# Performance work log

Measured on AMD Instinct MI355X. Metric: run time of the kernel, lower is better.

## Reference

```python
import jax, jax.numpy as jnp
import numpy as np
import math

B, S, DIM = 1, 2048, 1024
H, KVH = 16, 4
HD = DIM // H            # 64
KV_DIM = KVH * HD        # 256


def setup_inputs() -> dict:
    key = jax.random.key(0)
    ks = jax.random.split(key, 8)
    std = 0.02
    return {
        "x": jax.random.normal(ks[0], (B, S, DIM), jnp.float32),
        "Wq": jax.random.normal(ks[1], (DIM, DIM), jnp.float32) * std,
        "Wk": jax.random.normal(ks[2], (KV_DIM, DIM), jnp.float32) * std,
        "Wv": jax.random.normal(ks[3], (KV_DIM, DIM), jnp.float32) * std,
        "Wg": jax.random.normal(ks[4], (KV_DIM, DIM), jnp.float32) * std,
        "Wo": jax.random.normal(ks[5], (DIM, DIM), jnp.float32) * std,
        "q_gain": jnp.full((H,), 1.0, jnp.float32),
        "lambda_param": jnp.full((H,), 0.5, jnp.float32),
    }


def _rms_norm(x):
    eps = jnp.finfo(x.dtype).eps
    return x * jax.lax.rsqrt(jnp.mean(x * x, axis=-1, keepdims=True) + eps)


def _polar_rotary(seq_len, head_dim, dtype):
    # PolarRotary: angles = arange(0, d, 2)/d * pi; radius decays with position
    angles = jnp.arange(0, head_dim, 2, dtype=jnp.float32) / head_dim * math.pi
    pos = jnp.arange(seq_len, dtype=jnp.float32)
    radius = 1.0 / (1.0 + pos[:, None] * 0.01)          # [S, 1]
    ang = pos[:, None] * angles[None, :]                 # [S, d/2]
    cos = (radius * jnp.cos(ang)).astype(dtype)          # [S, d/2]
    sin = (radius * jnp.sin(ang)).astype(dtype)
    return cos[None, None], sin[None, None]              # [1,1,S,d/2]


def _apply_rotary(x, cos, sin):
    half = x.shape[-1] // 2
    x1, x2 = x[..., :half], x[..., half:]
    return jnp.concatenate([x1 * cos + x2 * sin, x1 * -sin + x2 * cos], axis=-1)


def _causal_attn(q, k, v, scale, mask):
    # q,k,v: [B,H,S,d]
    s = jnp.einsum("bhqd,bhkd->bhqk", q, k) * scale
    s = jnp.where(mask, s, jnp.finfo(s.dtype).min)
    p = jax.nn.softmax(s, axis=-1)
    return jnp.einsum("bhqk,bhkd->bhqd", p, v)


def reference(x, Wq, Wk, Wv, Wg, Wo, q_gain, lambda_param):
    bsz, seqlen, dim = x.shape
    q = (x @ Wq.T).reshape(bsz, seqlen, H, HD).transpose(0, 2, 1, 3)      # [B,H,S,d]
    k = (x @ Wk.T).reshape(bsz, seqlen, KVH, HD).transpose(0, 2, 1, 3)    # [B,KVH,S,d]
    v = (x @ Wv.T).reshape(bsz, seqlen, KVH, HD).transpose(0, 2, 1, 3)

    # value gate (VGA)
    v_g = jax.nn.sigmoid((x @ Wg.T).reshape(bsz, seqlen, KVH, HD).transpose(0, 2, 1, 3))
    v = v * v_g

    q = _rms_norm(q)
    k = _rms_norm(k)

    cos, sin = _polar_rotary(seqlen, HD, q.dtype)
    q = _apply_rotary(q, cos, sin)
    k = _apply_rotary(k, cos, sin)

    q = q * q_gain.astype(q.dtype)[None, :, None, None]

    # GQA: repeat kv heads
    rep = H // KVH
    k = jnp.repeat(k, rep, axis=1)
    v = jnp.repeat(v, rep, axis=1)

    # differential attention: split head dim in halves
    half = HD // 2
    q1, q2 = q[..., :half], q[..., half:]
    k1, k2 = k[..., :half], k[..., half:]
    v1, v2 = v[..., :half], v[..., half:]

    scale = 1.0 / math.sqrt(half)
    mask = jnp.tril(jnp.ones((seqlen, seqlen), dtype=bool))[None, None]
    a1 = _causal_attn(q1, k1, v1, scale, mask)
    a2 = _causal_attn(q2, k2, v2, scale, mask)

    lp = lambda_param.astype(q.dtype)[None, :, None, None]
    y = jnp.concatenate([a1 - lp * a2, a1 + lp * a2], axis=-1)            # [B,H,S,d]
    y = y.transpose(0, 2, 1, 3).reshape(bsz, seqlen, dim)
    return y @ Wo.T
```

## Files before the change

kernel.cpp:

```cpp
#include <hip/hip_runtime.h>
#include <hip/hip_bf16.h>
#include <math.h>

#define S_LEN 2048
#define DIM   1024
#define NH    16
#define NKVH  4
#define HD    64
#define KVDIM 256

typedef __hip_bfloat16 bf16;
typedef __attribute__((ext_vector_type(8))) short short8;
typedef __attribute__((ext_vector_type(4))) float f32x4;

#define GLOBAL_AS __attribute__((address_space(1)))
#define LDS_AS    __attribute__((address_space(3)))

__device__ __forceinline__ void gload_lds16(const bf16* g, bf16* l) {
    __builtin_amdgcn_global_load_lds((const GLOBAL_AS void*)g, (LDS_AS void*)l,
                                     16, 0, 0);
}

__global__ __launch_bounds__(256) void cast6(
    const float* __restrict__ x,  const float* __restrict__ Wq,
    const float* __restrict__ Wk, const float* __restrict__ Wv,
    const float* __restrict__ Wg, const float* __restrict__ Wo,
    bf16* __restrict__ xb,  bf16* __restrict__ Wqb,
    bf16* __restrict__ Wkb, bf16* __restrict__ Wvb,
    bf16* __restrict__ Wgb, bf16* __restrict__ Wob,
    float* __restrict__ rc, float* __restrict__ rs) {
    if (blockIdx.y == 6) {
        const int idx = blockIdx.x * 256 + threadIdx.x;
        if (idx < S_LEN * 32) {
            const int s = idx >> 5, i = idx & 31;
            float af  = (float)(((double)(2 * i) / 64.0) * 3.14159265358979323846);
            float ang = (float)s * af;
            float radius = 1.0f / (1.0f + 0.01f * (float)s);
            rc[idx] = radius * (float)cos((double)ang);
            rs[idx] = radius * (float)sin((double)ang);
        }
        return;
    }
    const float* s; bf16* d; int n;
    switch (blockIdx.y) {
        case 0: s = x;  d = xb;  n = S_LEN * DIM; break;
        case 1: s = Wq; d = Wqb; n = DIM * DIM;   break;
        case 2: s = Wk; d = Wkb; n = KVDIM * DIM; break;
        case 3: s = Wv; d = Wvb; n = KVDIM * DIM; break;
        case 4: s = Wg; d = Wgb; n = KVDIM * DIM; break;
        default: s = Wo; d = Wob; n = DIM * DIM;  break;
    }
    for (int i = (blockIdx.x * 256 + threadIdx.x) * 4; i < n; i += gridDim.x * 1024) {
        float4 v = *(const float4*)(s + i);
        d[i]     = __float2bfloat16(v.x);
        d[i + 1] = __float2bfloat16(v.y);
        d[i + 2] = __float2bfloat16(v.z);
        d[i + 3] = __float2bfloat16(v.w);
    }
}

__device__ __forceinline__ void gemm_core(
    const bf16* __restrict__ A, const bf16* __restrict__ B,
    float* __restrict__ C, int bm, int bn, int N, int K) {
    __shared__ bf16 As[64 * 64];
    __shared__ bf16 Bs[64 * 64];
    const int tid  = threadIdx.x;
    const int w    = tid >> 6;
    const int lane = tid & 63;
    const int quad = lane >> 4;
    const int lm   = lane & 15;
    const int srow = tid >> 3;
    const int sseg = (tid & 7) ^ (srow & 7);
    const bf16* a0p = A + (size_t)(bm + srow) * K + (sseg << 3);
    const bf16* a1p = a0p + (size_t)32 * K;
    const bf16* b0p = B + (size_t)(bn + srow) * K + (sseg << 3);
    const bf16* b1p = b0p + (size_t)32 * K;
    bf16* ldsA = As + w * 512;
    bf16* ldsB = Bs + w * 512;

    f32x4 acc[4] = {};
    const int ra  = w * 16 + lm;
    const int rax = ra & 7;
    const int aoff0 = ra * 64 + (((quad    ) ^ rax) << 3);
    const int aoff1 = ra * 64 + (((quad + 4) ^ rax) << 3);
    const int rbx = lm & 7;
    const int boff0 = lm * 64 + (((quad    ) ^ rbx) << 3);
    const int boff1 = lm * 64 + (((quad + 4) ^ rbx) << 3);

    for (int k0 = 0; k0 < K; k0 += 64) {
        gload_lds16(a0p + k0, ldsA);
        gload_lds16(a1p + k0, ldsA + 2048);
        gload_lds16(b0p + k0, ldsB);
        gload_lds16(b1p + k0, ldsB + 2048);
        __syncthreads();
        short8 a0 = *(const short8*)&As[aoff0];
        short8 a1 = *(const short8*)&As[aoff1];
        #pragma unroll
        for (int t = 0; t < 4; ++t) {
            short8 b0 = *(const short8*)&Bs[boff0 + t * 16 * 64];
            short8 b1 = *(const short8*)&Bs[boff1 + t * 16 * 64];
            acc[t] = __builtin_amdgcn_mfma_f32_16x16x32_bf16(a0, b0, acc[t], 0, 0, 0);
            acc[t] = __builtin_amdgcn_mfma_f32_16x16x32_bf16(a1, b1, acc[t], 0, 0, 0);
        }
        __syncthreads();
    }
    const int r0 = bm + w * 16 + quad * 4;
    #pragma unroll
    for (int t = 0; t < 4; ++t) {
        const int col = bn + t * 16 + lm;
        #pragma unroll
        for (int i = 0; i < 4; ++i)
            C[(size_t)(r0 + i) * N + col] = acc[t][i];
    }
}

__global__ __launch_bounds__(256) void gemm_out(
    const bf16* __restrict__ Yb, const bf16* __restrict__ Wob,
    float* __restrict__ C) {
    gemm_core(Yb, Wob, C, blockIdx.y * 64, blockIdx.x * 64, DIM, DIM);
}

__global__ __launch_bounds__(256) void gemm_qkvg_post(
    const bf16* __restrict__ xb,  const bf16* __restrict__ Wqb,
    const bf16* __restrict__ Wkb, const bf16* __restrict__ Wvb,
    const bf16* __restrict__ Wgb,
    bf16* __restrict__ Qb, bf16* __restrict__ Kpk, bf16* __restrict__ Vpk,
    const float* __restrict__ qgain,
    const float* __restrict__ rc, const float* __restrict__ rs) {
    __shared__ bf16 As[64 * 64];
    __shared__ bf16 Bs[64 * 64];
    __shared__ bf16 Gs[64 * 64];
    const int cx = blockIdx.x;
    const int bm = blockIdx.y * 64;
    const int tid  = threadIdx.x;
    const int w    = tid >> 6;
    const int lane = tid & 63;
    const int quad = lane >> 4;
    const int lm   = lane & 15;
    const int srow = tid >> 3;
    const int sseg = (tid & 7) ^ (srow & 7);

    int mode, bn;
    const bf16 *B0, *B1;
    if (cx < 4)      { mode = 2; bn = cx * 64;        B0 = Wvb; B1 = Wgb; }
    else if (cx < 8) { mode = 1; bn = (cx - 4) * 64;  B0 = Wkb; B1 = Wkb; }
    else             { mode = 0; bn = (cx - 8) * 64;  B0 = Wqb; B1 = Wqb; }

    const bf16* a0p = xb + (size_t)(bm + srow) * DIM + (sseg << 3);
    const bf16* a1p = a0p + (size_t)32 * DIM;
    const bf16* b0p = B0 + (size_t)(bn + srow) * DIM + (sseg << 3);
    const bf16* b1p = b0p + (size_t)32 * DIM;
    const bf16* g0p = B1 + (size_t)(bn + srow) * DIM + (sseg << 3);
    const bf16* g1p = g0p + (size_t)32 * DIM;
    bf16* ldsA = As + w * 512;
    bf16* ldsB = Bs + w * 512;
    bf16* ldsG = Gs + w * 512;

    f32x4 acc[4]  = {};
    f32x4 acc2[4] = {};
    const int ra  = w * 16 + lm;
    const int rax = ra & 7;
    const int aoff0 = ra * 64 + (((quad    ) ^ rax) << 3);
    const int aoff1 = ra * 64 + (((quad + 4) ^ rax) << 3);
    const int rbx = lm & 7;
    const int boff0 = lm * 64 + (((quad    ) ^ rbx) << 3);
    const int boff1 = lm * 64 + (((quad + 4) ^ rbx) << 3);

    for (int k0 = 0; k0 < DIM; k0 += 64) {
        gload_lds16(a0p + k0, ldsA);
        gload_lds16(a1p + k0, ldsA + 2048);
        gload_lds16(b0p + k0, ldsB);
        gload_lds16(b1p + k0, ldsB + 2048);
        if (mode == 2) {
            gload_lds16(g0p + k0, ldsG);
            gload_lds16(g1p + k0, ldsG + 2048);
        }
        __syncthreads();
        short8 a0 = *(const short8*)&As[aoff0];
        short8 a1 = *(const short8*)&As[aoff1];
        #pragma unroll
        for (int t = 0; t < 4; ++t) {
            short8 b0 = *(const short8*)&Bs[boff0 + t * 16 * 64];
            short8 b1 = *(const short8*)&Bs[boff1 + t * 16 * 64];
            acc[t] = __builtin_amdgcn_mfma_f32_16x16x32_bf16(a0, b0, acc[t], 0, 0, 0);
            acc[t] = __builtin_amdgcn_mfma_f32_16x16x32_bf16(a1, b1, acc[t], 0, 0, 0);
        }
        if (mode == 2) {
            #pragma unroll
            for (int t = 0; t < 4; ++t) {
                short8 g0 = *(const short8*)&Gs[boff0 + t * 16 * 64];
                short8 g1 = *(const short8*)&Gs[boff1 + t * 16 * 64];
                acc2[t] = __builtin_amdgcn_mfma_f32_16x16x32_bf16(a0, g0, acc2[t], 0, 0, 0);
                acc2[t] = __builtin_amdgcn_mfma_f32_16x16x32_bf16(a1, g1, acc2[t], 0, 0, 0);
            }
        }
        __syncthreads();
    }

    const int r0 = bm + w * 16 + quad * 4;
    if (mode == 2) {
        const int kvh = cx;
        #pragma unroll
        for (int t = 0; t < 4; ++t) {
            const int d = t * 16 + lm;
            const int half = d >> 5, d32 = d & 31;
            #pragma unroll
            for (int i = 0; i < 4; ++i) {
                const int s = r0 + i;
                float val = acc[t][i] / (1.0f + __expf(-acc2[t][i]));
                const size_t vi = (((((size_t)(kvh*2 + half)*64 + (s>>5))*2 + (d32>>4))*64)
                                   + ((s&31)>>3)*16 + (d32&15))*8 + (s&7);
                Vpk[vi] = __float2bfloat16(val);
            }
        }
    } else {
        const float gain = (mode == 0) ? qgain[cx - 8] : 1.0f;
        float rr[4];
        #pragma unroll
        for (int i = 0; i < 4; ++i) {
            float v0 = acc[0][i] * acc[0][i] + acc[2][i] * acc[2][i];
            float v1 = acc[1][i] * acc[1][i] + acc[3][i] * acc[3][i];
            float ssv = v0 + v1;
            ssv += __shfl_xor(ssv, 8);
            ssv += __shfl_xor(ssv, 4);
            ssv += __shfl_xor(ssv, 2);
            ssv += __shfl_xor(ssv, 1);
            rr[i] = rsqrtf(ssv * (1.0f/64.0f) + 1.1920928955078125e-7f);
        }
        #pragma unroll
        for (int t = 0; t < 4; ++t) {
            const int d = t * 16 + lm;
            #pragma unroll
            for (int i = 0; i < 4; ++i) {
                const int s = r0 + i;
                float n  = acc[t][i]     * rr[i];
                float no = acc[t ^ 2][i] * rr[i];
                const int ri = s * 32 + (d & 31);
                float c = rc[ri], sn = rs[ri];
                float val = (t < 2) ? (n * c + no * sn) * gain
                                    : (n * c + -no * sn) * gain;
                if (mode == 0) {
                    Qb[(size_t)s * DIM + (cx - 8) * 64 + d] = __float2bfloat16(val);
                } else {
                    const int kvh = cx - 4;
                    const int half = d >> 5, d32 = d & 31;
                    const size_t ki = (((((size_t)(kvh*2 + half)*64 + (s>>5))*2 + ((s&31)>>4))*64)
                                       + (d32>>3)*16 + (s&15))*8 + (d32&7);
                    Kpk[ki] = __float2bfloat16(val);
                }
            }
        }
    }
}

__global__ __launch_bounds__(64, 4) void attn_mfma(
    const bf16* __restrict__ Qb, const bf16* __restrict__ Kpk,
    const bf16* __restrict__ Vpk, float* __restrict__ Ao) {
    __shared__ short PW[640];
    const int id    = blockIdx.x;
    const int qtile = 127 - (id >> 5);
    const int hh    = id & 31;
    const int h     = hh >> 1;
    const int half  = hh & 1;
    const int kvh   = h >> 2;
    const int lane  = threadIdx.x;
    const int quad  = lane >> 4;
    const int m     = lane & 15;
    bf16* PWb = (bf16*)PW;

    const int qrow = qtile * 16 + m;
    short8 qf = *(const short8*)(Qb + (size_t)qrow * DIM + h * HD + half * 32 + quad * 8);

    const bf16* kbase = Kpk + (size_t)(kvh * 2 + half) * 64 * 1024 + lane * 8;
    const bf16* vbase = Vpk + (size_t)(kvh * 2 + half) * 64 * 1024 + lane * 8;

    f32x4 o0 = {}, o1 = {};
    float lpart[4] = {0.f, 0.f, 0.f, 0.f};
    const float scale = 0.17677669529663687f;
    const int rbase = qtile * 16 + quad * 4;
    const int nkt = (qtile >> 1) + 1;

    for (int kb = 0; kb < nkt; ++kb) {
        short8 kf0 = *(const short8*)(kbase + kb * 1024);
        short8 kf1 = *(const short8*)(kbase + kb * 1024 + 512);
        f32x4 s0 = {}, s1 = {};
        s0 = __builtin_amdgcn_mfma_f32_16x16x32_bf16(qf, kf0, s0, 0, 0, 0);
        s1 = __builtin_amdgcn_mfma_f32_16x16x32_bf16(qf, kf1, s1, 0, 0, 0);
        short8 vtf0 = *(const short8*)(vbase + kb * 1024);
        short8 vtf1 = *(const short8*)(vbase + kb * 1024 + 512);
        const int kg = kb * 32 + m;
        #pragma unroll
        for (int r = 0; r < 4; ++r) {
            const int rg = rbase + r;
            const float p0 = (kg > rg)      ? 0.f : __expf(s0[r] * scale);
            const float p1 = (kg + 16 > rg) ? 0.f : __expf(s1[r] * scale);
            lpart[r] += p0 + p1;
            PWb[(quad * 4 + r) * 40 + m]      = __float2bfloat16(p0);
            PWb[(quad * 4 + r) * 40 + 16 + m] = __float2bfloat16(p1);
        }
        asm volatile("s_waitcnt lgkmcnt(0)" ::: "memory");
        short8 pf = *(const short8*)&PW[m * 40 + quad * 8];
        o0 = __builtin_amdgcn_mfma_f32_16x16x32_bf16(pf, vtf0, o0, 0, 0, 0);
        o1 = __builtin_amdgcn_mfma_f32_16x16x32_bf16(pf, vtf1, o1, 0, 0, 0);
    }

    #pragma unroll
    for (int r = 0; r < 4; ++r) {
        float v = lpart[r];
        v += __shfl_xor(v, 1);
        v += __shfl_xor(v, 2);
        v += __shfl_xor(v, 4);
        v += __shfl_xor(v, 8);
        lpart[r] = 1.f / v;
    }
    #pragma unroll
    for (int r = 0; r < 4; ++r) {
        float* op = Ao + (size_t)(rbase + r) * DIM + h * HD + half * 32;
        op[m]      = o0[r] * lpart[r];
        op[16 + m] = o1[r] * lpart[r];
    }
}

__global__ __launch_bounds__(256) void combine_kernel(
    const float* __restrict__ A, const float* __restrict__ lambda_p,
    bf16* __restrict__ Y) {
    const int idx = blockIdx.x * 256 + threadIdx.x;
    const int c = idx & (DIM - 1);
    const int s = idx >> 10;
    const int hh = c >> 6;
    const int d = c & 63;
    const float* base = A + (size_t)s * DIM + hh * HD;
    const float lam = lambda_p[hh];
    float y;
    if (d < 32) y = base[d]      - lam * base[d + 32];
    else        y = base[d - 32] + lam * base[d];
    Y[idx] = __float2bfloat16(y);
}

extern "C" void kernel_launch(void* const* d_in, const int* in_sizes, int n_in,
                              void* d_out, int out_size, void* d_ws, size_t ws_size,
                              hipStream_t stream) {
    const float* x  = (const float*)d_in[0];
    const float* Wq = (const float*)d_in[1];
    const float* Wk = (const float*)d_in[2];
    const float* Wv = (const float*)d_in[3];
    const float* Wg = (const float*)d_in[4];
    const float* Wo = (const float*)d_in[5];
    const float* qg = (const float*)d_in[6];
    const float* lp = (const float*)d_in[7];
    float* out = (float*)d_out;

    char* ws = (char*)d_ws;
    bf16* Qb   = (bf16*)ws;
    bf16* Kpk  = (bf16*)(ws + (8u << 20));
    bf16* Vpk  = (bf16*)(ws + (9u << 20));
    float* rc  = (float*)(ws + (14u << 20));
    float* rs  = (float*)(ws + (14u << 20) + (256u << 10));
    float* Ao  = (float*)(ws + (14u << 20));
    bf16* xb   = (bf16*)(ws + (22u << 20));
    bf16* Wqb  = (bf16*)(ws + (26u << 20));
    bf16* Wkb  = (bf16*)(ws + (28u << 20));
    bf16* Wvb  = (bf16*)(ws + (28u << 20) + (512u << 10));
    bf16* Wgb  = (bf16*)(ws + (29u << 20));
    bf16* Wob  = (bf16*)(ws + (29u << 20) + (512u << 10));
    bf16* Yb   = (bf16*)ws;

    cast6<<<dim3(512, 7), 256, 0, stream>>>(x, Wq, Wk, Wv, Wg, Wo,
                                            xb, Wqb, Wkb, Wvb, Wgb, Wob, rc, rs);

    gemm_qkvg_post<<<dim3(24, S_LEN/64), 256, 0, stream>>>(
        xb, Wqb, Wkb, Wvb, Wgb, Qb, Kpk, Vpk, qg, rc, rs);

    attn_mfma<<<4096, 64, 0, stream>>>(Qb, Kpk, Vpk, Ao);

    combine_kernel<<<S_LEN * DIM / 256, 256, 0, stream>>>(Ao, lp, Yb);

    gemm_out<<<dim3(DIM/64, S_LEN/64), 256, 0, stream>>>(Yb, Wob, out);
}
```

Baseline: 149.3 us.

## Fold differential-attention combine into Wo and process two q-tiles per attention block

```diff
diff --git a/kernel.cpp b/kernel.cpp
--- a/kernel.cpp
+++ b/kernel.cpp
@@ -28,7 +28,8 @@
     bf16* __restrict__ xb,  bf16* __restrict__ Wqb,
     bf16* __restrict__ Wkb, bf16* __restrict__ Wvb,
     bf16* __restrict__ Wgb, bf16* __restrict__ Wob,
-    float* __restrict__ rc, float* __restrict__ rs) {
+    float* __restrict__ rc, float* __restrict__ rs,
+    const float* __restrict__ lp) {
     if (blockIdx.y == 6) {
         const int idx = blockIdx.x * 256 + threadIdx.x;
         if (idx < S_LEN * 32) {
@@ -41,14 +42,37 @@
         }
         return;
     }
+    if (blockIdx.y == 5) {
+        for (int i = (blockIdx.x * 256 + threadIdx.x) * 4; i < DIM * DIM;
+             i += gridDim.x * 1024) {
+            const int n = i >> 10, c = i & (DIM - 1);
+            const int h = c >> 6, half = (c >> 5) & 1, d = c & 31;
+            const float* base = Wo + (size_t)n * DIM + h * 64 + d;
+            float4 w1 = *(const float4*)(base);
+            float4 w2 = *(const float4*)(base + 32);
+            const float lam = lp[h];
+            float4 r;
+            if (half == 0) {
+                r.x = w1.x + w2.x; r.y = w1.y + w2.y;
+                r.z = w1.z + w2.z; r.w = w1.w + w2.w;
+            } else {
+                r.x = lam * (w2.x - w1.x); r.y = lam * (w2.y - w1.y);
+                r.z = lam * (w2.z - w1.z); r.w = lam * (w2.w - w1.w);
+            }
+            Wob[i]     = __float2bfloat16(r.x);
+            Wob[i + 1] = __float2bfloat16(r.y);
+            Wob[i + 2] = __float2bfloat16(r.z);
+            Wob[i + 3] = __float2bfloat16(r.w);
+        }
+        return;
+    }
     const float* s; bf16* d; int n;
     switch (blockIdx.y) {
         case 0: s = x;  d = xb;  n = S_LEN * DIM; break;
         case 1: s = Wq; d = Wqb; n = DIM * DIM;   break;
         case 2: s = Wk; d = Wkb; n = KVDIM * DIM; break;
         case 3: s = Wv; d = Wvb; n = KVDIM * DIM; break;
-        case 4: s = Wg; d = Wgb; n = KVDIM * DIM; break;
-        default: s = Wo; d = Wob; n = DIM * DIM;  break;
+        default: s = Wg; d = Wgb; n = KVDIM * DIM; break;
     }
     for (int i = (blockIdx.x * 256 + threadIdx.x) * 4; i < n; i += gridDim.x * 1024) {
         float4 v = *(const float4*)(s + i);
@@ -253,12 +277,12 @@
     }
 }
 
-__global__ __launch_bounds__(64, 4) void attn_mfma(
+__global__ __launch_bounds__(64, 2) void attn_mfma(
     const bf16* __restrict__ Qb, const bf16* __restrict__ Kpk,
-    const bf16* __restrict__ Vpk, float* __restrict__ Ao) {
-    __shared__ short PW[640];
+    const bf16* __restrict__ Vpk, bf16* __restrict__ Yab) {
+    __shared__ short PW[1280];
     const int id    = blockIdx.x;
-    const int qtile = 127 - (id >> 5);
+    const int qg    = 63 - (id >> 5);
     const int hh    = id & 31;
     const int h     = hh >> 1;
     const int half  = hh & 1;
@@ -266,75 +290,87 @@
     const int lane  = threadIdx.x;
     const int quad  = lane >> 4;
     const int m     = lane & 15;
-    bf16* PWb = (bf16*)PW;
-
-    const int qrow = qtile * 16 + m;
-    short8 qf = *(const short8*)(Qb + (size_t)qrow * DIM + h * HD + half * 32 + quad * 8);
+    bf16* PWa = (bf16*)PW;
+    bf16* PWb = (bf16*)(PW + 640);
+
+    const int qta = qg * 2, qtb = qg * 2 + 1;
+    short8 qfa = *(const short8*)(Qb + (size_t)(qta * 16 + m) * DIM + h * HD + half * 32 + quad * 8);
+    short8 qfb = *(const short8*)(Qb + (size_t)(qtb * 16 + m) * DIM + h * HD + half * 32 + quad * 8);
 
     const bf16* kbase = Kpk + (size_t)(kvh * 2 + half) * 64 * 1024 + lane * 8;
     const bf16* vbase = Vpk + (size_t)(kvh * 2 + half) * 64 * 1024 + lane * 8;
 
-    f32x4 o0 = {}, o1 = {};
-    float lpart[4] = {0.f, 0.f, 0.f, 0.f};
+    f32x4 o0a = {}, o1a = {}, o0b = {}, o1b = {};
+    float lpa[4] = {0.f, 0.f, 0.f, 0.f};
+    float lpb[4] = {0.f, 0.f, 0.f, 0.f};
     const float scale = 0.17677669529663687f;
-    const int rbase = qtile * 16 + quad * 4;
-    const int nkt = (qtile >> 1) + 1;
+    const int rba = qta * 16 + quad * 4;
+    const int rbb = qtb * 16 + quad * 4;
+    const int nkt = qg + 1;
+
+    short8 kf0 = *(const short8*)(kbase);
+    short8 kf1 = *(const short8*)(kbase + 512);
+    short8 vt0 = *(const short8*)(vbase);
+    short8 vt1 = *(const short8*)(vbase + 512);
 
     for (int kb = 0; kb < nkt; ++kb) {
-        short8 kf0 = *(const short8*)(kbase + kb * 1024);
-        short8 kf1 = *(const short8*)(kbase + kb * 1024 + 512);
-        f32x4 s0 = {}, s1 = {};
-        s0 = __builtin_amdgcn_mfma_f32_16x16x32_bf16(qf, kf0, s0, 0, 0, 0);
-        s1 = __builtin_amdgcn_mfma_f32_16x16x32_bf16(qf, kf1, s1, 0, 0, 0);
-        short8 vtf0 = *(const short8*)(vbase + kb * 1024);
-        short8 vtf1 = *(const short8*)(vbase + kb * 1024 + 512);
+        const int kn = (kb + 1 < nkt) ? kb + 1 : kb;
+        short8 nk0 = *(const short8*)(kbase + kn * 1024);
+        short8 nk1 = *(const short8*)(kbase + kn * 1024 + 512);
+        short8 nv0 = *(const short8*)(vbase + kn * 1024);
+        short8 nv1 = *(const short8*)(vbase + kn * 1024 + 512);
+
+        f32x4 s0a = {}, s1a = {}, s0b = {}, s1b = {};
+        s0a = __builtin_amdgcn_mfma_f32_16x16x32_bf16(qfa, kf0, s0a, 0, 0, 0);
+        s1a = __builtin_amdgcn_mfma_f32_16x16x32_bf16(qfa, kf1, s1a, 0, 0, 0);
+        s0b = __builtin_amdgcn_mfma_f32_16x16x32_bf16(qfb, kf0, s0b, 0, 0, 0);
+        s1b = __builtin_amdgcn_mfma_f32_16x16x32_bf16(qfb, kf1, s1b, 0, 0, 0);
+
         const int kg = kb * 32 + m;
         #pragma unroll
         for (int r = 0; r < 4; ++r) {
-            const int rg = rbase + r;
-            const float p0 = (kg > rg)      ? 0.f : __expf(s0[r] * scale);
-            const float p1 = (kg + 16 > rg) ? 0.f : __expf(s1[r] * scale);
-            lpart[r] += p0 + p1;
-            PWb[(quad * 4 + r) * 40 + m]      = __float2bfloat16(p0);
-            PWb[(quad * 4 + r) * 40 + 16 + m] = __float2bfloat16(p1);
+            const int rga = rba + r;
+            const float p0a = (kg > rga)      ? 0.f : __expf(s0a[r] * scale);
+            const float p1a = (kg + 16 > rga) ? 0.f : __expf(s1a[r] * scale);
+            lpa[r] += p0a + p1a;
+            PWa[(quad * 4 + r) * 40 + m]      = __float2bfloat16(p0a);
+            PWa[(quad * 4 + r) * 40 + 16 + m] = __float2bfloat16(p1a);
+            const int rgb = rbb + r;
+            const float p0b = (kg > rgb)      ? 0.f : __expf(s0b[r] * scale);
+            const float p1b = (kg + 16 > rgb) ? 0.f : __expf(s1b[r] * scale);
+            lpb[r] += p0b + p1b;
+            PWb[(quad * 4 + r) * 40 + m]      = __float2bfloat16(p0b);
+            PWb[(quad * 4 + r) * 40 + 16 + m] = __float2bfloat16(p1b);
         }
         asm volatile("s_waitcnt lgkmcnt(0)" ::: "memory");
-        short8 pf = *(const short8*)&PW[m * 40 + quad * 8];
-        o0 = __builtin_amdgcn_mfma_f32_16x16x32_bf16(pf, vtf0, o0, 0, 0, 0);
-        o1 = __builtin_amdgcn_mfma_f32_16x16x32_bf16(pf, vtf1, o1, 0, 0, 0);
+        short8 pfa = *(const short8*)&PWa[m * 40 + quad * 8];
+        short8 pfb = *(const short8*)&PWb[m * 40 + quad * 8];
+        o0a = __builtin_amdgcn_mfma_f32_16x16x32_bf16(pfa, vt0, o0a, 0, 0, 0);
+        o1a = __builtin_amdgcn_mfma_f32_16x16x32_bf16(pfa, vt1, o1a, 0, 0, 0);
+        o0b = __builtin_amdgcn_mfma_f32_16x16x32_bf16(pfb, vt0, o0b, 0, 0, 0);
+        o1b = __builtin_amdgcn_mfma_f32_16x16x32_bf16(pfb, vt1, o1b, 0, 0, 0);
+
+        kf0 = nk0; kf1 = nk1; vt0 = nv0; vt1 = nv1;
     }
 
     #pragma unroll
     for (int r = 0; r < 4; ++r) {
-        float v = lpart[r];
-        v += __shfl_xor(v, 1);
-        v += __shfl_xor(v, 2);
-        v += __shfl_xor(v, 4);
-        v += __shfl_xor(v, 8);
-        lpart[r] = 1.f / v;
+        float va = lpa[r], vb = lpb[r];
+        va += __shfl_xor(va, 1); vb += __shfl_xor(vb, 1);
+        va += __shfl_xor(va, 2); vb += __shfl_xor(vb, 2);
+        va += __shfl_xor(va, 4); vb += __shfl_xor(vb, 4);
+        va += __shfl_xor(va, 8); vb += __shfl_xor(vb, 8);
+        lpa[r] = 1.f / va; lpb[r] = 1.f / vb;
     }
     #pragma unroll
     for (int r = 0; r < 4; ++r) {
-        float* op = Ao + (size_t)(rbase + r) * DIM + h * HD + half * 32;
-        op[m]      = o0[r] * lpart[r];
-        op[16 + m] = o1[r] * lpart[r];
-    }
-}
-
-__global__ __launch_bounds__(256) void combine_kernel(
-    const float* __restrict__ A, const float* __restrict__ lambda_p,
-    bf16* __restrict__ Y) {
-    const int idx = blockIdx.x * 256 + threadIdx.x;
-    const int c = idx & (DIM - 1);
-    const int s = idx >> 10;
-    const int hh = c >> 6;
-    const int d = c & 63;
-    const float* base = A + (size_t)s * DIM + hh * HD;
-    const float lam = lambda_p[hh];
-    float y;
-    if (d < 32) y = base[d]      - lam * base[d + 32];
-    else        y = base[d - 32] + lam * base[d];
-    Y[idx] = __float2bfloat16(y);
+        bf16* opa = Yab + (size_t)(rba + r) * DIM + h * HD + half * 32;
+        bf16* opb = Yab + (size_t)(rbb + r) * DIM + h * HD + half * 32;
+        opa[m]      = __float2bfloat16(o0a[r] * lpa[r]);
+        opa[16 + m] = __float2bfloat16(o1a[r] * lpa[r]);
+        opb[m]      = __float2bfloat16(o0b[r] * lpb[r]);
+        opb[16 + m] = __float2bfloat16(o1b[r] * lpb[r]);
+    }
 }
 
 extern "C" void kernel_launch(void* const* d_in, const int* in_sizes, int n_in,
@@ -356,24 +392,22 @@
     bf16* Vpk  = (bf16*)(ws + (9u << 20));
     float* rc  = (float*)(ws + (14u << 20));
     float* rs  = (float*)(ws + (14u << 20) + (256u << 10));
-    float* Ao  = (float*)(ws + (14u << 20));
+    bf16* Yab  = (bf16*)(ws + (14u << 20));
     bf16* xb   = (bf16*)(ws + (22u << 20));
     bf16* Wqb  = (bf16*)(ws + (26u << 20));
     bf16* Wkb  = (bf16*)(ws + (28u << 20));
     bf16* Wvb  = (bf16*)(ws + (28u << 20) + (512u << 10));
     bf16* Wgb  = (bf16*)(ws + (29u << 20));
     bf16* Wob  = (bf16*)(ws + (29u << 20) + (512u << 10));
-    bf16* Yb   = (bf16*)ws;
 
     cast6<<<dim3(512, 7), 256, 0, stream>>>(x, Wq, Wk, Wv, Wg, Wo,
-                                            xb, Wqb, Wkb, Wvb, Wgb, Wob, rc, rs);
+                                            xb, Wqb, Wkb, Wvb, Wgb, Wob,
+                                            rc, rs, lp);
 
     gemm_qkvg_post<<<dim3(24, S_LEN/64), 256, 0, stream>>>(
         xb, Wqb, Wkb, Wvb, Wgb, Qb, Kpk, Vpk, qg, rc, rs);
 
-    attn_mfma<<<4096, 64, 0, stream>>>(Qb, Kpk, Vpk, Ao);
-
-    combine_kernel<<<S_LEN * DIM / 256, 256, 0, stream>>>(Ao, lp, Yb);
-
-    gemm_out<<<dim3(DIM/64, S_LEN/64), 256, 0, stream>>>(Yb, Wob, out);
-}
+    attn_mfma<<<2048, 64, 0, stream>>>(Qb, Kpk, Vpk, Yab);
+
+    gemm_out<<<dim3(DIM/64, S_LEN/64), 256, 0, stream>>>(Yab, Wob, out);
+}
```

Measured after the change: 150.3 us. About the same (+0.7%).

## Fold differential-attention combine into Wo and split attention KV loop across four waves

Applied to the files above, without the earlier changes.

```diff
diff --git a/kernel.cpp b/kernel.cpp
--- a/kernel.cpp
+++ b/kernel.cpp
@@ -28,7 +28,8 @@
     bf16* __restrict__ xb,  bf16* __restrict__ Wqb,
     bf16* __restrict__ Wkb, bf16* __restrict__ Wvb,
     bf16* __restrict__ Wgb, bf16* __restrict__ Wob,
-    float* __restrict__ rc, float* __restrict__ rs) {
+    float* __restrict__ rc, float* __restrict__ rs,
+    const float* __restrict__ lp) {
     if (blockIdx.y == 6) {
         const int idx = blockIdx.x * 256 + threadIdx.x;
         if (idx < S_LEN * 32) {
@@ -41,14 +42,37 @@
         }
         return;
     }
+    if (blockIdx.y == 5) {
+        for (int i = (blockIdx.x * 256 + threadIdx.x) * 4; i < DIM * DIM;
+             i += gridDim.x * 1024) {
+            const int n = i >> 10, c = i & (DIM - 1);
+            const int h = c >> 6, half = (c >> 5) & 1, d = c & 31;
+            const float* base = Wo + (size_t)n * DIM + h * 64 + d;
+            float4 w1 = *(const float4*)(base);
+            float4 w2 = *(const float4*)(base + 32);
+            const float lam = lp[h];
+            float4 r;
+            if (half == 0) {
+                r.x = w1.x + w2.x; r.y = w1.y + w2.y;
+                r.z = w1.z + w2.z; r.w = w1.w + w2.w;
+            } else {
+                r.x = lam * (w2.x - w1.x); r.y = lam * (w2.y - w1.y);
+                r.z = lam * (w2.z - w1.z); r.w = lam * (w2.w - w1.w);
+            }
+            Wob[i]     = __float2bfloat16(r.x);
+            Wob[i + 1] = __float2bfloat16(r.y);
+            Wob[i + 2] = __float2bfloat16(r.z);
+            Wob[i + 3] = __float2bfloat16(r.w);
+        }
+        return;
+    }
     const float* s; bf16* d; int n;
     switch (blockIdx.y) {
         case 0: s = x;  d = xb;  n = S_LEN * DIM; break;
         case 1: s = Wq; d = Wqb; n = DIM * DIM;   break;
         case 2: s = Wk; d = Wkb; n = KVDIM * DIM; break;
         case 3: s = Wv; d = Wvb; n = KVDIM * DIM; break;
-        case 4: s = Wg; d = Wgb; n = KVDIM * DIM; break;
-        default: s = Wo; d = Wob; n = DIM * DIM;  break;
+        default: s = Wg; d = Wgb; n = KVDIM * DIM; break;
     }
     for (int i = (blockIdx.x * 256 + threadIdx.x) * 4; i < n; i += gridDim.x * 1024) {
         float4 v = *(const float4*)(s + i);
@@ -253,20 +277,23 @@
     }
 }
 
-__global__ __launch_bounds__(64, 4) void attn_mfma(
+__global__ __launch_bounds__(256, 8) void attn_mfma(
     const bf16* __restrict__ Qb, const bf16* __restrict__ Kpk,
-    const bf16* __restrict__ Vpk, float* __restrict__ Ao) {
-    __shared__ short PW[640];
+    const bf16* __restrict__ Vpk, bf16* __restrict__ Yab) {
+    __shared__ short PW[4][640];
+    __shared__ float RED[3][64][13];
     const int id    = blockIdx.x;
     const int qtile = 127 - (id >> 5);
     const int hh    = id & 31;
     const int h     = hh >> 1;
     const int half  = hh & 1;
     const int kvh   = h >> 2;
-    const int lane  = threadIdx.x;
+    const int tid   = threadIdx.x;
+    const int wid   = tid >> 6;
+    const int lane  = tid & 63;
     const int quad  = lane >> 4;
     const int m     = lane & 15;
-    bf16* PWb = (bf16*)PW;
+    bf16* PWb = (bf16*)PW[wid];
 
     const int qrow = qtile * 16 + m;
     short8 qf = *(const short8*)(Qb + (size_t)qrow * DIM + h * HD + half * 32 + quad * 8);
@@ -280,14 +307,14 @@
     const int rbase = qtile * 16 + quad * 4;
     const int nkt = (qtile >> 1) + 1;
 
-    for (int kb = 0; kb < nkt; ++kb) {
+    for (int kb = wid; kb < nkt; kb += 4) {
         short8 kf0 = *(const short8*)(kbase + kb * 1024);
         short8 kf1 = *(const short8*)(kbase + kb * 1024 + 512);
         f32x4 s0 = {}, s1 = {};
         s0 = __builtin_amdgcn_mfma_f32_16x16x32_bf16(qf, kf0, s0, 0, 0, 0);
         s1 = __builtin_amdgcn_mfma_f32_16x16x32_bf16(qf, kf1, s1, 0, 0, 0);
-        short8 vtf0 = *(const short8*)(vbase + kb * 1024);
-        short8 vtf1 = *(const short8*)(vbase + kb * 1024 + 512);
+        short8 vt0 = *(const short8*)(vbase + kb * 1024);
+        short8 vt1 = *(const short8*)(vbase + kb * 1024 + 512);
         const int kg = kb * 32 + m;
         #pragma unroll
         for (int r = 0; r < 4; ++r) {
@@ -299,42 +326,48 @@
             PWb[(quad * 4 + r) * 40 + 16 + m] = __float2bfloat16(p1);
         }
         asm volatile("s_waitcnt lgkmcnt(0)" ::: "memory");
-        short8 pf = *(const short8*)&PW[m * 40 + quad * 8];
-        o0 = __builtin_amdgcn_mfma_f32_16x16x32_bf16(pf, vtf0, o0, 0, 0, 0);
-        o1 = __builtin_amdgcn_mfma_f32_16x16x32_bf16(pf, vtf1, o1, 0, 0, 0);
-    }
-
-    #pragma unroll
-    for (int r = 0; r < 4; ++r) {
-        float v = lpart[r];
-        v += __shfl_xor(v, 1);
-        v += __shfl_xor(v, 2);
-        v += __shfl_xor(v, 4);
-        v += __shfl_xor(v, 8);
-        lpart[r] = 1.f / v;
-    }
-    #pragma unroll
-    for (int r = 0; r < 4; ++r) {
-        float* op = Ao + (size_t)(rbase + r) * DIM + h * HD + half * 32;
-        op[m]      = o0[r] * lpart[r];
-        op[16 + m] = o1[r] * lpart[r];
-    }
-}
-
-__global__ __launch_bounds__(256) void combine_kernel(
-    const float* __restrict__ A, const float* __restrict__ lambda_p,
-    bf16* __restrict__ Y) {
-    const int idx = blockIdx.x * 256 + threadIdx.x;
-    const int c = idx & (DIM - 1);
-    const int s = idx >> 10;
-    const int hh = c >> 6;
-    const int d = c & 63;
-    const float* base = A + (size_t)s * DIM + hh * HD;
-    const float lam = lambda_p[hh];
-    float y;
-    if (d < 32) y = base[d]      - lam * base[d + 32];
-    else        y = base[d - 32] + lam * base[d];
-    Y[idx] = __float2bfloat16(y);
+        short8 pf = *(const short8*)&PW[wid][m * 40 + quad * 8];
+        o0 = __builtin_amdgcn_mfma_f32_16x16x32_bf16(pf, vt0, o0, 0, 0, 0);
+        o1 = __builtin_amdgcn_mfma_f32_16x16x32_bf16(pf, vt1, o1, 0, 0, 0);
+    }
+
+    if (wid > 0) {
+        float* rp = &RED[wid - 1][lane][0];
+        #pragma unroll
+        for (int r = 0; r < 4; ++r) {
+            rp[r]     = o0[r];
+            rp[4 + r] = o1[r];
+            rp[8 + r] = lpart[r];
+        }
+    }
+    __syncthreads();
+    if (wid == 0) {
+        #pragma unroll
+        for (int wv = 0; wv < 3; ++wv) {
+            const float* rp = &RED[wv][lane][0];
+            #pragma unroll
+            for (int r = 0; r < 4; ++r) {
+                o0[r]     += rp[r];
+                o1[r]     += rp[4 + r];
+                lpart[r]  += rp[8 + r];
+            }
+        }
+        #pragma unroll
+        for (int r = 0; r < 4; ++r) {
+            float v = lpart[r];
+            v += __shfl_xor(v, 1);
+            v += __shfl_xor(v, 2);
+            v += __shfl_xor(v, 4);
+            v += __shfl_xor(v, 8);
+            lpart[r] = 1.f / v;
+        }
+        #pragma unroll
+        for (int r = 0; r < 4; ++r) {
+            bf16* op = Yab + (size_t)(rbase + r) * DIM + h * HD + half * 32;
+            op[m]      = __float2bfloat16(o0[r] * lpart[r]);
+            op[16 + m] = __float2bfloat16(o1[r] * lpart[r]);
+        }
+    }
 }
 
 extern "C" void kernel_launch(void* const* d_in, const int* in_sizes, int n_in,
@@ -356,24 +389,22 @@
     bf16* Vpk  = (bf16*)(ws + (9u << 20));
     float* rc  = (float*)(ws + (14u << 20));
     float* rs  = (float*)(ws + (14u << 20) + (256u << 10));
-    float* Ao  = (float*)(ws + (14u << 20));
+    bf16* Yab  = (bf16*)(ws + (14u << 20));
     bf16* xb   = (bf16*)(ws + (22u << 20));
     bf16* Wqb  = (bf16*)(ws + (26u << 20));
     bf16* Wkb  = (bf16*)(ws + (28u << 20));
     bf16* Wvb  = (bf16*)(ws + (28u << 20) + (512u << 10));
     bf16* Wgb  = (bf16*)(ws + (29u << 20));
     bf16* Wob  = (bf16*)(ws + (29u << 20) + (512u << 10));
-    bf16* Yb   = (bf16*)ws;
 
     cast6<<<dim3(512, 7), 256, 0, stream>>>(x, Wq, Wk, Wv, Wg, Wo,
-                                            xb, Wqb, Wkb, Wvb, Wgb, Wob, rc, rs);
+                                            xb, Wqb, Wkb, Wvb, Wgb, Wob,
+                                            rc, rs, lp);
 
     gemm_qkvg_post<<<dim3(24, S_LEN/64), 256, 0, stream>>>(
         xb, Wqb, Wkb, Wvb, Wgb, Qb, Kpk, Vpk, qg, rc, rs);
 
-    attn_mfma<<<4096, 64, 0, stream>>>(Qb, Kpk, Vpk, Ao);
-
-    combine_kernel<<<S_LEN * DIM / 256, 256, 0, stream>>>(Ao, lp, Yb);
-
-    gemm_out<<<dim3(DIM/64, S_LEN/64), 256, 0, stream>>>(Yb, Wob, out);
-}
+    attn_mfma<<<4096, 256, 0, stream>>>(Qb, Kpk, Vpk, Yab);
+
+    gemm_out<<<dim3(DIM/64, S_LEN/64), 256, 0, stream>>>(Yab, Wob, out);
+}
```

Result: faster. 131.1 us (-12.2%).
